# Optimization experiments

Hardware: AMD Instinct MI355X
Metric: run time of the kernel (lower is better)

## Reference

```python
import jax, jax.numpy as jnp
import numpy as np

NUM_EXPERTS = 8
INPUT_SIZE = 2048
OUTPUT_SIZE = 8192
EXPERT_SIZES = np.array([3000, 5000, 4096, 2048, 6000, 4000, 4624, 4000], dtype=np.int64)  # sums to 32768
TOTAL_TOKENS = int(EXPERT_SIZES.sum())


def setup_inputs() -> dict:
    key = jax.random.key(0)
    k_in, k_w = jax.random.split(key)
    inputs = jax.random.normal(k_in, (TOTAL_TOKENS, INPUT_SIZE), dtype=jnp.float32)
    # per-expert Linear weights, torch layout [out, in]
    weights = jax.random.normal(k_w, (NUM_EXPERTS, OUTPUT_SIZE, INPUT_SIZE), dtype=jnp.float32) * 0.02
    expert_size = jnp.asarray(EXPERT_SIZES)
    return {"inputs": inputs, "weights": weights, "expert_size": expert_size}


def reference(inputs, weights, expert_size):
    # Grouped GEMM: split tokens by static per-expert counts, y_i = x_i @ W_i^T, concat.
    sizes = [int(s) for s in np.asarray(expert_size)]
    offsets = np.concatenate([[0], np.cumsum(sizes)])
    outs = []
    for i in range(len(sizes)):
        x_i = inputs[offsets[i]:offsets[i + 1]]  # [n_i, input_size]
        outs.append(jnp.einsum('ti,oi->to', x_i, weights[i]))  # [n_i, output_size]
    return jnp.concatenate(outs, axis=0)  # [total_tokens, output_size]
```

## Files before the change

### kernel.cpp

```cpp
#include <hip/hip_runtime.h>

typedef __bf16 bf16x8 __attribute__((ext_vector_type(8)));
typedef float  f32x4  __attribute__((ext_vector_type(4)));

#define KDIM 2048
#define NDIM 8192
#define MTOT 32768
#define BM 256
#define BN 256
#define BK 64
#define NT 32
#define NMT 131
#define NWG (NMT * 32)
#define ABUF (BM * BK)
#define BBUF (BN * BK)

__device__ __forceinline__ void gload_lds16(const void* g, void* l) {
    __builtin_amdgcn_global_load_lds(
        (const __attribute__((address_space(1))) void*)g,
        (__attribute__((address_space(3))) void*)l, 16, 0, 0);
}

__global__ __launch_bounds__(256) void convert_f32_bf16(
    const float* __restrict__ src, __bf16* __restrict__ dst, int n8)
{
    const int stride = gridDim.x * blockDim.x;
    for (int i = blockIdx.x * blockDim.x + threadIdx.x; i < n8; i += stride) {
        const f32x4* p = (const f32x4*)(src + (size_t)i * 8);
        f32x4 a = p[0], b = p[1];
        bf16x8 h;
        #pragma unroll
        for (int j = 0; j < 4; ++j) { h[j] = (__bf16)a[j]; h[4 + j] = (__bf16)b[j]; }
        *(bf16x8*)(dst + (size_t)i * 8) = h;
    }
}

__global__ void __launch_bounds__(512, 2) moe_gemm_3a(
    const __bf16* __restrict__ A,
    const __bf16* __restrict__ W,
    float* __restrict__ C)
{
    __shared__ __bf16 AsF[3 * ABUF];
    __shared__ __bf16 BsF[2 * BBUF];

    const int tstart[9] = {0, 12, 32, 48, 56, 80, 96, 115, 131};
    const int offs[9]   = {0, 3000, 8000, 12096, 14144, 20144, 24144, 28768, 32768};

    const int bid = blockIdx.x;
    const int mt = bid >> 5;
    const int nt = bid & 31;

    int e = 0;
    #pragma unroll
    for (int i = 1; i < 8; ++i) e += (mt >= tstart[i]) ? 1 : 0;
    const int row0 = offs[e] + (mt - tstart[e]) * BM;
    int rows = offs[e + 1] - row0;
    if (rows > BM) rows = BM;
    const int col0 = nt * BN;

    const int tid  = threadIdx.x;
    const int lane = tid & 63;
    const int w    = tid >> 6;
    const int wm   = w >> 2;
    const int wn   = w & 3;

    const int lrow = lane >> 3;
    const int csrc = ((lane & 7) ^ lrow) * 8;

    const __bf16 *aX[2], *aY[2], *b0[2], *b1[2];
    int ldsAX[2], ldsAY[2], ldsB0[2], ldsB1[2];
    #pragma unroll
    for (int c = 0; c < 2; ++c) {
        const int q  = w * 2 + c;
        const int tX = q * 8 + (q & 8) * 8;
        const int tY = tX + 64;
        int rX = tX + lrow; rX = (rX < rows) ? rX : 0;
        int rY = tY + lrow; rY = (rY < rows) ? rY : 0;
        aX[c] = A + (size_t)(row0 + rX) * KDIM + csrc;
        aY[c] = A + (size_t)(row0 + rY) * KDIM + csrc;
        b0[c] = W + (size_t)(e * NDIM + col0 + q * 8 + lrow) * KDIM + csrc;
        b1[c] = W + (size_t)(e * NDIM + col0 + 128 + q * 8 + lrow) * KDIM + csrc;
        ldsAX[c] = tX * BK;
        ldsAY[c] = tY * BK;
        ldsB0[c] = (q * 8) * BK;
        ldsB1[c] = (128 + q * 8) * BK;
    }

#define STAGE_A(ab, o) { \
    gload_lds16(aX[0] + (o), &AsF[(ab) * ABUF + ldsAX[0]]); \
    gload_lds16(aX[1] + (o), &AsF[(ab) * ABUF + ldsAX[1]]); \
    gload_lds16(aY[0] + (o), &AsF[(ab) * ABUF + ldsAY[0]]); \
    gload_lds16(aY[1] + (o), &AsF[(ab) * ABUF + ldsAY[1]]); }
#define STAGE_B(bb, o) { \
    gload_lds16(b0[0] + (o), &BsF[(bb) * BBUF + ldsB0[0]]); \
    gload_lds16(b0[1] + (o), &BsF[(bb) * BBUF + ldsB0[1]]); \
    gload_lds16(b1[0] + (o), &BsF[(bb) * BBUF + ldsB1[0]]); \
    gload_lds16(b1[1] + (o), &BsF[(bb) * BBUF + ldsB1[1]]); }

    const int frow = lane & 15;
    const int g8   = (lane >> 4) * 8;
    const int swc  = (frow & 7) << 3;
    const int ck0  = g8 ^ swc;
    const int ck1  = (32 + g8) ^ swc;
    const int arow = wm * 128 + frow;
    const int brow = wn * 64 + frow;

    f32x4 acc[8][4];
    #pragma unroll
    for (int m = 0; m < 8; ++m)
        #pragma unroll
        for (int n = 0; n < 4; ++n)
            acc[m][n] = (f32x4){0.f, 0.f, 0.f, 0.f};

    bf16x8 bk0[4], bk1[4];
    bf16x8 av0[4], av1[4];

#define RD_B(bb) { _Pragma("unroll") for (int n = 0; n < 4; ++n) { \
        bk0[n] = *(const bf16x8*)&BsF[(bb) * BBUF + (brow + n * 16) * BK + ck0]; \
        bk1[n] = *(const bf16x8*)&BsF[(bb) * BBUF + (brow + n * 16) * BK + ck1]; } }

#define RD_A(ab, h) { _Pragma("unroll") for (int mm = 0; mm < 4; ++mm) { \
        av0[mm] = *(const bf16x8*)&AsF[(ab) * ABUF + (arow + (4 * (h) + mm) * 16) * BK + ck0]; \
        av1[mm] = *(const bf16x8*)&AsF[(ab) * ABUF + (arow + (4 * (h) + mm) * 16) * BK + ck1]; } }

#define MFMA_CL(h) { \
    __builtin_amdgcn_s_setprio(1); \
    _Pragma("unroll") for (int mm = 0; mm < 4; ++mm) \
        _Pragma("unroll") for (int n = 0; n < 4; ++n) \
            acc[4 * (h) + mm][n] = __builtin_amdgcn_mfma_f32_16x16x32_bf16( \
                av0[mm], bk0[n], acc[4 * (h) + mm][n], 0, 0, 0); \
    _Pragma("unroll") for (int mm = 0; mm < 4; ++mm) \
        _Pragma("unroll") for (int n = 0; n < 4; ++n) \
            acc[4 * (h) + mm][n] = __builtin_amdgcn_mfma_f32_16x16x32_bf16( \
                av1[mm], bk1[n], acc[4 * (h) + mm][n], 0, 0, 0); \
    __builtin_amdgcn_s_setprio(0); }

#define FENCE asm volatile("" ::: "memory")

    STAGE_A(0, 0); STAGE_B(0, 0);
    STAGE_A(1, BK); STAGE_B(1, BK);
    asm volatile("s_waitcnt vmcnt(8)" ::: "memory");
    __builtin_amdgcn_s_barrier();

    int a0 = 0;
    #pragma unroll 1
    for (int i = 0; i < 16; ++i) {
        int a1 = a0 + 1; if (a1 >= 3) a1 -= 3;
        int a2 = a0 + 2; if (a2 >= 3) a2 -= 3;
        int t2 = 2 * i + 2; if (t2 > NT - 1) t2 = NT - 1;
        int t3 = 2 * i + 3; if (t3 > NT - 1) t3 = NT - 1;
        const int t2o = t2 * BK;
        const int t3o = t3 * BK;

        FENCE;
        RD_B(0);
        RD_A(a0, 0);
        STAGE_A(a2, t2o);
        MFMA_CL(0);
        __builtin_amdgcn_s_barrier();

        FENCE;
        RD_A(a0, 1);
        STAGE_B(0, t2o);
        MFMA_CL(1);
        asm volatile("s_waitcnt vmcnt(8)" ::: "memory");
        __builtin_amdgcn_s_barrier();

        FENCE;
        RD_B(1);
        RD_A(a1, 0);
        STAGE_A(a0, t3o);
        MFMA_CL(0);
        __builtin_amdgcn_s_barrier();

        FENCE;
        RD_A(a1, 1);
        STAGE_B(1, t3o);
        MFMA_CL(1);
        asm volatile("s_waitcnt vmcnt(8)" ::: "memory");
        __builtin_amdgcn_s_barrier();

        a0 = a2;
    }

    const int crow = (lane >> 4) * 4;
    const int ccol = lane & 15;
    #pragma unroll
    for (int m = 0; m < 8; ++m) {
        #pragma unroll
        for (int j2 = 0; j2 < 4; ++j2) {
            const int r = wm * 128 + m * 16 + crow + j2;
            if (r < rows) {
                float* dst = C + (size_t)(row0 + r) * NDIM + col0 + wn * 64 + ccol;
                #pragma unroll
                for (int n = 0; n < 4; ++n)
                    dst[n * 16] = acc[m][n][j2];
            }
        }
    }
#undef STAGE_A
#undef STAGE_B
#undef RD_B
#undef RD_A
#undef MFMA_CL
#undef FENCE
}

__global__ __launch_bounds__(256) void moe_gemm_f32(
    const float* __restrict__ A, const float* __restrict__ W, float* __restrict__ C)
{
    __shared__ __bf16 Asb[128][64];
    __shared__ __bf16 Bsb[128][64];

    const int tstart[9] = {0, 24, 64, 96, 112, 159, 191, 228, 260};
    const int offs[9]   = {0, 3000, 8000, 12096, 14144, 20144, 24144, 28768, 32768};

    const int mt = blockIdx.y;
    int e = 0;
    #pragma unroll
    for (int i = 1; i < 8; ++i) e += (mt >= tstart[i]) ? 1 : 0;
    const int row0 = offs[e] + (mt - tstart[e]) * 128;
    int rows = offs[e + 1] - row0;
    if (rows > 128) rows = 128;
    const int col0 = blockIdx.x * 128;

    const float* __restrict__ Abase = A + (size_t)row0 * KDIM;
    const float* __restrict__ Wbase = W + ((size_t)e * NDIM + (size_t)col0) * KDIM;

    const int tid  = threadIdx.x;
    const int lane = tid & 63;
    const int wid  = tid >> 6;
    const int wr   = (wid >> 1) * 64;
    const int wc   = (wid & 1) * 64;
    const int srow = tid >> 2;
    const int scol = (tid & 3) * 16;

    f32x4 acc[4][4];
    #pragma unroll
    for (int m = 0; m < 4; ++m)
        #pragma unroll
        for (int n = 0; n < 4; ++n)
            acc[m][n] = (f32x4){0.f, 0.f, 0.f, 0.f};
    const f32x4 fzero = (f32x4){0.f, 0.f, 0.f, 0.f};

    for (int k0 = 0; k0 < KDIM; k0 += 64) {
        __syncthreads();
        #pragma unroll
        for (int rr = 0; rr < 2; ++rr) {
            const int r = srow + rr * 64;
            {
                const bool valid = (r < rows);
                const float* pa = Abase + (size_t)r * KDIM + k0 + scol;
                f32x4 v[4];
                #pragma unroll
                for (int i = 0; i < 4; ++i) v[i] = valid ? *(const f32x4*)(pa + 4 * i) : fzero;
                bf16x8 h0, h1;
                #pragma unroll
                for (int i = 0; i < 8; ++i) {
                    h0[i] = (__bf16)v[i >> 2][i & 3];
                    h1[i] = (__bf16)v[2 + (i >> 2)][i & 3];
                }
                *((bf16x8*)&Asb[r][scol]) = h0;
                *((bf16x8*)&Asb[r][scol + 8]) = h1;
            }
            {
                const float* pb = Wbase + (size_t)r * KDIM + k0 + scol;
                f32x4 v[4];
                #pragma unroll
                for (int i = 0; i < 4; ++i) v[i] = *(const f32x4*)(pb + 4 * i);
                bf16x8 h0, h1;
                #pragma unroll
                for (int i = 0; i < 8; ++i) {
                    h0[i] = (__bf16)v[i >> 2][i & 3];
                    h1[i] = (__bf16)v[2 + (i >> 2)][i & 3];
                }
                *((bf16x8*)&Bsb[r][scol]) = h0;
                *((bf16x8*)&Bsb[r][scol + 8]) = h1;
            }
        }
        __syncthreads();
        #pragma unroll
        for (int ks = 0; ks < 2; ++ks) {
            const int kb = ks * 32 + (lane >> 4) * 8;
            bf16x8 af[4], bfr[4];
            #pragma unroll
            for (int m = 0; m < 4; ++m)
                af[m] = *((const bf16x8*)&Asb[wr + m * 16 + (lane & 15)][kb]);
            #pragma unroll
            for (int n = 0; n < 4; ++n)
                bfr[n] = *((const bf16x8*)&Bsb[wc + n * 16 + (lane & 15)][kb]);
            #pragma unroll
            for (int m = 0; m < 4; ++m)
                #pragma unroll
                for (int n = 0; n < 4; ++n)
                    acc[m][n] = __builtin_amdgcn_mfma_f32_16x16x32_bf16(
                        af[m], bfr[n], acc[m][n], 0, 0, 0);
        }
    }

    const int crow = (lane >> 4) * 4;
    const int ccol = lane & 15;
    #pragma unroll
    for (int m = 0; m < 4; ++m) {
        #pragma unroll
        for (int j = 0; j < 4; ++j) {
            const int r = wr + m * 16 + crow + j;
            if (r < rows) {
                float* dst = C + (size_t)(row0 + r) * NDIM + col0 + wc + ccol;
                #pragma unroll
                for (int n = 0; n < 4; ++n)
                    dst[n * 16] = acc[m][n][j];
            }
        }
    }
}

extern "C" void kernel_launch(void* const* d_in, const int* in_sizes, int n_in,
                              void* d_out, int out_size, void* d_ws, size_t ws_size,
                              hipStream_t stream) {
    const float* A = (const float*)d_in[0];
    const float* W = (const float*)d_in[1];
    float* C = (float*)d_out;

    const size_t nA = (size_t)MTOT * KDIM;
    const size_t nW = (size_t)8 * NDIM * KDIM;
    const size_t WS_NEED = (nA + nW) * 2;

    if (ws_size >= WS_NEED) {
        __bf16* Abf = (__bf16*)d_ws;
        __bf16* Wbf = (__bf16*)((char*)d_ws + nA * 2);
        hipLaunchKernelGGL(convert_f32_bf16, dim3(2048), dim3(256), 0, stream,
                           A, Abf, (int)(nA / 8));
        hipLaunchKernelGGL(convert_f32_bf16, dim3(2048), dim3(256), 0, stream,
                           W, Wbf, (int)(nW / 8));
        hipLaunchKernelGGL(moe_gemm_3a, dim3(NWG), dim3(512), 0, stream,
                           Abf, Wbf, C);
    } else {
        hipLaunchKernelGGL(moe_gemm_f32, dim3(NDIM / 128, 260), dim3(256), 0, stream,
                           A, W, C);
    }
}
```

Before: 1.430 ms.

## Restructure GEMM main loop to one barrier per K tile

Rewrites the software pipeline of the bf16 grouped GEMM main loop. Each iteration now handles one K tile: it stages B one tile ahead into a double buffer and A two tiles ahead into a triple buffer, runs both MFMA halves, then waits and hits a single barrier. The old loop took two K tiles per iteration with four barriers. The aim is to cut barrier and synchronisation overhead, at the cost of a shorter prefetch distance for B, which may expose more global-load latency.

```diff
diff --git a/kernel.cpp b/kernel.cpp
--- a/kernel.cpp
+++ b/kernel.cpp
@@ -35,7 +35,7 @@
     }
 }
 
-__global__ void __launch_bounds__(512, 2) moe_gemm_3a(
+__global__ void __launch_bounds__(512, 2) moe_gemm_1b(
     const __bf16* __restrict__ A,
     const __bf16* __restrict__ W,
     float* __restrict__ C)
@@ -138,49 +138,31 @@
 #define FENCE asm volatile("" ::: "memory")
 
     STAGE_A(0, 0); STAGE_B(0, 0);
-    STAGE_A(1, BK); STAGE_B(1, BK);
-    asm volatile("s_waitcnt vmcnt(8)" ::: "memory");
+    STAGE_A(1, BK);
+    asm volatile("s_waitcnt vmcnt(4)" ::: "memory");
     __builtin_amdgcn_s_barrier();
 
-    int a0 = 0;
+    int a0i = 0;
+    int b0i = 0;
     #pragma unroll 1
-    for (int i = 0; i < 16; ++i) {
-        int a1 = a0 + 1; if (a1 >= 3) a1 -= 3;
-        int a2 = a0 + 2; if (a2 >= 3) a2 -= 3;
-        int t2 = 2 * i + 2; if (t2 > NT - 1) t2 = NT - 1;
-        int t3 = 2 * i + 3; if (t3 > NT - 1) t3 = NT - 1;
-        const int t2o = t2 * BK;
-        const int t3o = t3 * BK;
+    for (int i = 0; i < NT; ++i) {
+        int a2i = a0i + 2; if (a2i >= 3) a2i -= 3;
+        int t1 = i + 1; if (t1 > NT - 1) t1 = NT - 1;
+        int t2 = i + 2; if (t2 > NT - 1) t2 = NT - 1;
 
         FENCE;
-        RD_B(0);
-        RD_A(a0, 0);
-        STAGE_A(a2, t2o);
+        RD_B(b0i);
+        RD_A(a0i, 0);
+        STAGE_B(b0i ^ 1, t1 * BK);
+        STAGE_A(a2i, t2 * BK);
         MFMA_CL(0);
+        RD_A(a0i, 1);
+        MFMA_CL(1);
+        asm volatile("s_waitcnt vmcnt(4)" ::: "memory");
         __builtin_amdgcn_s_barrier();
 
-        FENCE;
-        RD_A(a0, 1);
-        STAGE_B(0, t2o);
-        MFMA_CL(1);
-        asm volatile("s_waitcnt vmcnt(8)" ::: "memory");
-        __builtin_amdgcn_s_barrier();
-
-        FENCE;
-        RD_B(1);
-        RD_A(a1, 0);
-        STAGE_A(a0, t3o);
-        MFMA_CL(0);
-        __builtin_amdgcn_s_barrier();
-
-        FENCE;
-        RD_A(a1, 1);
-        STAGE_B(1, t3o);
-        MFMA_CL(1);
-        asm volatile("s_waitcnt vmcnt(8)" ::: "memory");
-        __builtin_amdgcn_s_barrier();
-
-        a0 = a2;
+        a0i = a0i + 1; if (a0i >= 3) a0i -= 3;
+        b0i ^= 1;
     }
 
     const int crow = (lane >> 4) * 4;
@@ -333,7 +315,7 @@
                            A, Abf, (int)(nA / 8));
         hipLaunchKernelGGL(convert_f32_bf16, dim3(2048), dim3(256), 0, stream,
                            W, Wbf, (int)(nW / 8));
-        hipLaunchKernelGGL(moe_gemm_3a, dim3(NWG), dim3(512), 0, stream,
+        hipLaunchKernelGGL(moe_gemm_1b, dim3(NWG), dim3(512), 0, stream,
                            Abf, Wbf, C);
     } else {
         hipLaunchKernelGGL(moe_gemm_f32, dim3(NDIM / 128, 260), dim3(256), 0, stream,
```

New measurement: 1.434 ms. No clear change (+0.3%).
